# Performance work log

Measured on AMD Instinct MI355X. Metric: run time of the kernel, lower is better.

Reference implementation:

```python
import jax, jax.numpy as jnp
import numpy as np

N = 1147      # 240 lncRNA + 412 disease + 495 miRNA nodes (hard-coded in source)
HID = 512
NH = 8        # heads
P = 73408     # edges (avg degree ~64)
IN_CH = 512


def _ln(x, eps=1e-5):
    m = x.mean(-1, keepdims=True)
    v = ((x - m) ** 2).mean(-1, keepdims=True)
    return (x - m) * jax.lax.rsqrt(v + eps)


def _seg_softmax_agg(logits, v_src, dst, n):
    # logits: [P, NH], v_src: [P, NH, d]; softmax over incoming edges per dst node
    m = jax.ops.segment_max(logits, dst, num_segments=n)
    m = jnp.where(jnp.isfinite(m), m, 0.0)
    a = jnp.exp(logits - m[dst])
    den = jax.ops.segment_sum(a, dst, num_segments=n)
    w = a / (den[dst] + 1e-9)
    return jax.ops.segment_sum(w[..., None] * v_src, dst, num_segments=n)


def _lap_pe(src, dst, n, k):
    # symmetric normalized Laplacian eigenvector positional encoding
    A = jnp.zeros((n, n), jnp.float32).at[src, dst].set(1.0)
    A = jnp.maximum(A, A.T)
    dinv = jax.lax.rsqrt(jnp.maximum(A.sum(1), 1.0))
    L = jnp.eye(n, dtype=jnp.float32) - dinv[:, None] * A * dinv[None, :]
    _, vecs = jnp.linalg.eigh(L)
    return vecs[:, 1:k + 1]  # drop trivial eigenvector


def _edge_layer(h, e, src, dst, Wq, Wk, Wv, We, Wo, Woe, Wfa, Wfb, Wea, Web):
    n, D = h.shape
    d = D // NH
    scale = 1.0 / np.sqrt(d)
    q = (h @ Wq).reshape(n, NH, d)
    k = (h @ Wk).reshape(n, NH, d)
    v = (h @ Wv).reshape(n, NH, d)
    ep = (e @ We).reshape(-1, NH, d)
    score = k[src] * q[dst] * scale * ep           # [P, NH, d]
    e1 = _ln(e + score.reshape(-1, D) @ Woe)       # edge residual path
    e1 = _ln(e1 + jax.nn.relu(e1 @ Wea) @ Web)
    agg = _seg_softmax_agg(score.sum(-1), v[src], dst, n).reshape(n, D)
    h1 = _ln(h + agg @ Wo)
    h1 = _ln(h1 + jax.nn.relu(h1 @ Wfa) @ Wfb)
    return h1, e1


def _gt_layer(h, src, dst, Wq, Wk, Wv, Wo, Wfa, Wfb):
    n, D = h.shape
    d = D // NH
    scale = 1.0 / np.sqrt(d)
    q = (h @ Wq).reshape(n, NH, d)
    k = (h @ Wk).reshape(n, NH, d)
    v = (h @ Wv).reshape(n, NH, d)
    logits = (k[src] * q[dst]).sum(-1) * scale     # [P, NH]
    agg = _seg_softmax_agg(logits, v[src], dst, n).reshape(n, D)
    h1 = _ln(h + agg @ Wo)
    h1 = _ln(h1 + jax.nn.relu(h1 @ Wfa) @ Wfb)
    return h1


def setup_inputs() -> dict:
    key = jax.random.key(0)
    ks = jax.random.split(key, 32)
    s = 0.02
    w = lambda i, shp: jax.random.normal(ks[i], shp, jnp.float32) * s
    return {
        'H': jax.random.normal(ks[0], (N, 1147), jnp.float32),
        'edge_w': jax.random.uniform(ks[1], (P, 1), jnp.float32),
        'edge_src': jax.random.randint(ks[2], (P,), 0, N, jnp.int32),
        'edge_dst': jax.random.randint(ks[3], (P,), 0, N, jnp.int32),
        'W_lin': w(4, (1147, IN_CH)), 'b_lin': jnp.zeros((IN_CH,), jnp.float32),
        'W_e': w(5, (1, HID)), 'b_e': jnp.zeros((HID,), jnp.float32),
        'W_h': w(6, (IN_CH, HID)), 'b_h': jnp.zeros((HID,), jnp.float32),
        'W_lap': w(7, (HID, HID)), 'b_lap': jnp.zeros((HID,), jnp.float32),
        'Wq1': w(8, (HID, HID)), 'Wk1': w(9, (HID, HID)), 'Wv1': w(10, (HID, HID)),
        'We1': w(11, (HID, HID)), 'Wo1': w(12, (HID, HID)), 'Woe1': w(13, (HID, HID)),
        'Wf1a': w(14, (HID, 2 * HID)), 'Wf1b': w(15, (2 * HID, HID)),
        'We1a': w(16, (HID, 2 * HID)), 'We1b': w(17, (2 * HID, HID)),
        'Wq2': w(18, (HID, HID)), 'Wk2': w(19, (HID, HID)), 'Wv2': w(20, (HID, HID)),
        'Wo2': w(21, (HID, HID)),
        'Wf2a': w(22, (HID, 2 * HID)), 'Wf2b': w(23, (2 * HID, HID)),
    }


def reference(H, edge_w, W_lin, b_lin, W_e, b_e, W_h, b_h, W_lap, b_lap,
              Wq1, Wk1, Wv1, We1, Wo1, Woe1, Wf1a, Wf1b, We1a, We1b,
              Wq2, Wk2, Wv2, Wo2, Wf2a, Wf2b, edge_src, edge_dst):
    e = edge_w @ W_e + b_e                       # embedding_e on edge weights
    h = (H @ W_lin + b_lin) @ W_h + b_h          # linear(1147->in_ch) then embedding_h
    pe = _lap_pe(edge_src, edge_dst, N, HID)     # laplacian positional encoding
    h = h + pe @ W_lap + b_lap
    z, _ = _edge_layer(h, e, edge_src, edge_dst, Wq1, Wk1, Wv1, We1,
                       Wo1, Woe1, Wf1a, Wf1b, We1a, We1b)
    z = _gt_layer(z, edge_src, edge_dst, Wq2, Wk2, Wv2, Wo2, Wf2a, Wf2b)
    return z  # [N, HID], already flat per node
```

## Files before the change

### kernel.cpp

```cpp
#include <hip/hip_runtime.h>
#include <hip/hip_cooperative_groups.h>
#include <math.h>

#define NN 1147
#define HID 512
#define LDAe 1152
#define LDQ 1152
#define LDD 1147
#define EPS32 5.9604644775390625e-08f
#define SAFMIN32 1.17549435e-38f
#define I0E 1026
#define TGRID 64
#define TBLK 1024
#define GENSTRIDE 16

struct EDMeta { int K; int nrot; int early; float rho; };
struct ETree { int st[64]; int sz[64]; int cnt; };
struct MergeLvl { int cnt; int st[32]; int n1[32]; int n2[32]; };

__device__ __forceinline__ float lapy2f(float x, float y){
  float xa=fabsf(x), ya=fabsf(y), w=fmaxf(xa,ya), z2=fminf(xa,ya);
  if (z2==0.f) return w;
  float q=z2/w; return w*sqrtf(1.f+q*q);
}
// ... 88 lines not shown
  size_t idx=(size_t)row*LDAe+col;
  float v=A[idx];
  float v1=(dinv[row]*v)*dinv[col];
  float v2=(dinv[col]*v)*dinv[row];
  A[idx] = ((row==col)?1.f:0.f) - 0.5f*(v1+v2);
}

__device__ __forceinline__ float dload(const float* p){
  return __hip_atomic_load(p, __ATOMIC_RELAXED, __HIP_MEMORY_SCOPE_AGENT);
}
__device__ __forceinline__ void dstore(float* p, float v){
  __hip_atomic_store(p, v, __ATOMIC_RELAXED, __HIP_MEMORY_SCOPE_AGENT);
}

__device__ __forceinline__ void gbar(unsigned* flags, unsigned* genrep, unsigned tgt){
  __syncthreads();
  if (threadIdx.x==0)
    __hip_atomic_store(&flags[blockIdx.x], tgt, __ATOMIC_RELAXED, __HIP_MEMORY_SCOPE_AGENT);
  if (blockIdx.x==0){
    if (threadIdx.x<TGRID){
      while (__hip_atomic_load(&flags[threadIdx.x], __ATOMIC_RELAXED, __HIP_MEMORY_SCOPE_AGENT) < tgt)
        __builtin_amdgcn_s_sleep(1);
    }
    __syncthreads();
    if (threadIdx.x<TGRID)
      __hip_atomic_store(&genrep[threadIdx.x*GENSTRIDE], tgt, __ATOMIC_RELAXED, __HIP_MEMORY_SCOPE_AGENT);
  } else {
    if (threadIdx.x==0){
      while (__hip_atomic_load(&genrep[blockIdx.x*GENSTRIDE], __ATOMIC_RELAXED, __HIP_MEMORY_SCOPE_AGENT) < tgt)
        __builtin_amdgcn_s_sleep(1);
    }
    __syncthreads();
  }
}

__global__ __launch_bounds__(1024) void k_trid(float* __restrict__ A, float* __restrict__ evec,
    float* __restrict__ tauv, float* __restrict__ scalv, float* __restrict__ pv2,
    float* __restrict__ pub4, unsigned* __restrict__ flags, unsigned* __restrict__ genrep){
  __shared__ float vbuf[2][1152];
  __shared__ float pcur[1152];
  __shared__ float pubc[1152];
  __shared__ float red[256];
  __shared__ float bcv;
  int tid=threadIdx.x, bid=blockIdx.x;
  int wv=tid>>6, lane=tid&63;
  unsigned tgt=0;
  float tau, scal;
  {
    const float* row0=A;
    int m0=NN-1;
    if (tid<256){
      float s=0.f;
      for(int t=tid;t<m0-1;t+=256){ float x=row0[2+t]; s+=x*x; }
      red[tid]=s;
    }
    float xn2=tree256(red,&bcv,tid);
    float alpha=row0[1];
    float beta;
    if(xn2==0.f){ tau=0.f; beta=alpha; scal=0.f; }
    else { beta=-copysignf(sqrtf(alpha*alpha+xn2),alpha); tau=(beta-alpha)/beta; scal=1.f/(alpha-beta); }
    if(bid==0&&tid==0){ evec[0]=beta; tauv[0]=tau; scalv[0]=scal; }
    for(int t=tid;t<m0;t+=TBLK) vbuf[0][t]=row0[1+t];
    __syncthreads();
    for(int rr=0;rr<2;rr++){
      int r=16*bid+wv+rr*1024;
      if(r<1||r>=NN) continue;
      const float* arow=A+(size_t)r*LDAe+1;
      float acc=0.f;
      for(int c=lane;c<m0;c+=64){
        float v=(c==0)?1.f:vbuf[0][c]*scal;
        acc+=arow[c]*v;
      }
      for(int o=32;o;o>>=1) acc+=__shfl_down(acc,o,64);
      if(lane==0) dstore(&pv2[r],acc);
    }
    if(bid==0&&wv==1){
      const float* r1=A+(size_t)LDAe;
      for(int c=2+lane;c<NN;c+=64) dstore(&pub4[1280+c],r1[c]);
    }
  }
  gbar(flags,genrep,++tgt);
  int cur=0;
  for(int i=0;i<I0E;i++){
    int m=NN-1-i, mp=m-1;
    float* vcur=vbuf[cur]; float* nxt=vbuf[cur^1];
    const float* pvs=pv2+(size_t)(i&1)*1280;
    const float* pbs=pub4+(size_t)((i+1)&3)*1280;
    if (tid<256){
      float s=0.f;
      for(int t=tid;t<m;t+=256){
        float pv=dload(&pvs[(i+1)+t]);
        pcur[t]=pv;
        float v=(t==0)?1.f:vcur[t]*scal;
        s+=pv*v;
      }
      red[tid]=s;
    } else {
      for(int t=tid-256;t<mp;t+=768) pubc[t]=dload(&pbs[(i+2)+t]);
    }
    float sv=tree256(red,&bcv,tid);
    float c2=tau*tau*sv*0.5f;
    const float vz=1.f;
    float wR0=tau*pcur[0]-c2*vz;
    if (tid<256){
      float s2=0.f;
      if (tid==0){
        float vC=vcur[1]*scal;
        float wC=tau*pcur[1]-c2*vC;
        nxt[0]=pubc[0]-(vz*wC+wR0*vC);
      }
      for(int u=tid+1;u<mp;u+=256){
        float vC=vcur[1+u]*scal;
        float wC=tau*pcur[1+u]-c2*vC;
        float x=pubc[u]-(vz*wC+wR0*vC);
        nxt[u]=x;
        s2+=x*x;
      }
      red[tid]=s2;
    }
    float xn2=tree256(red,&bcv,tid);
    float alpha1=nxt[0];
    float beta1,tau1,scal1;
    if(xn2==0.f){ tau1=0.f; beta1=alpha1; scal1=0.f; }
    else { beta1=-copysignf(sqrtf(alpha1*alpha1+xn2),alpha1); tau1=(beta1-alpha1)/beta1; scal1=1.f/(alpha1-beta1); }
    if(bid==0&&tid==0){ evec[i+1]=beta1; tauv[i+1]=tau1; scalv[i+1]=scal1; }
    float* pvd=pv2+(size_t)((i+1)&1)*1280;
    float* pbd=pub4+(size_t)((i+2)&3)*1280;
    for(int rr=0;rr<2;rr++){
      int r=16*bid+wv+rr*1024;
      if(r<i+1||r>=NN) continue;
      int tr=r-(i+1);
      float vR=(tr==0)?1.f:vcur[tr]*scal;
      float wR=tau*pcur[tr]-c2*vR;
      float* arow=A+(size_t)r*LDAe;
      if(lane==0) arow[i+1]=arow[i+1]-(vR*wR0+wR*vz);
      if(tr==0){
        for(int c=lane;c<mp;c+=64) arow[i+2+c]=nxt[c];
      } else {
        float acc=0.f;
        int ispub=(tr==1);
        for(int c=lane;c<mp;c+=64){
          float vC=vcur[1+c]*scal;
          float wC=tau*pcur[1+c]-c2*vC;
          float val=arow[i+2+c]-(vR*wC+wR*vC);
          arow[i+2+c]=val;
          float v1=(c==0)?1.f:nxt[c]*scal1;
          acc+=val*v1;
          if(ispub) dstore(&pbd[(i+2)+c],val);
        }
        for(int o=32;o;o>>=1) acc+=__shfl_down(acc,o,64);
        if(lane==0) dstore(&pvd[r],acc);
      }
    }
    gbar(flags,genrep,++tgt);
    cur^=1; tau=tau1; scal=scal1;
  }
}
__global__ __launch_bounds__(256) void k_tend(float* __restrict__ A, float* __restrict__ evec,
    float* __restrict__ tauv, float* __restrict__ scalv){
  __shared__ float T[121][122];
  __shared__ float red[256];
  __shared__ float bct;
  __shared__ float pl[121];
  __shared__ float el[121], tl[121], sl[121];
  __shared__ float sh3[2];
  int tid=threadIdx.x;
// ... 136 lines not shown
        for(int j2=mm-1;j2>=l;j2--){
          float cc=workc[j2-l], ss2=works[j2-l];
          if (cc!=1.f||ss2!=0.f)
            for(int row=lane;row<n;row+=64){
              float t1=z[(size_t)(j2+1)*ldz+row];
              z[(size_t)(j2+1)*ldz+row]=cc*t1 - ss2*z[(size_t)j2*ldz+row];
              z[(size_t)j2*ldz+row]=ss2*t1 + cc*z[(size_t)j2*ldz+row];
            }
        }
        d[l]=d[l]-p;
        e[l]=g;
      }
    } else {
      for(;;){
        int mm;
        for(mm=l;mm>lend;mm--){
          float tst=e[mm-1]*e[mm-1];
          if (tst<=(eps2*fabsf(d[mm]))*fabsf(d[mm-1])+safmin) break;
        }
        if (mm>lend) e[mm-1]=0.f;
        p=d[l];
        if (mm==l){ d[l]=p; l--; if (l>=lend) continue; else break; }
        if (mm==l-1){
          slaev2(d[l-1],e[l-1],d[l],&rt1,&rt2,&c,&s);
          for(int row=lane;row<n;row+=64){
            float t1=z[(size_t)l*ldz+row];
            z[(size_t)l*ldz+row]=c*t1 - s*z[(size_t)(l-1)*ldz+row];
            z[(size_t)(l-1)*ldz+row]=s*t1 + c*z[(size_t)(l-1)*ldz+row];
          }
          d[l-1]=rt1; d[l]=rt2; e[l-1]=0.f;
          l-=2;
          if (l>=lend) continue; else break;
        }
        if (jtot==nmaxit) break;
        jtot++;
        g=(d[l-1]-p)/(2.f*e[l-1]);
        r=lapy2f(g,1.f);
        g=d[mm]-p+(e[l-1]/(g+copysignf(r,g)));
        s=1.f; c=1.f; p=0.f;
        for(int i=mm;i<=l-1;i++){
          f=s*e[i]; b=c*e[i];
          slartg(g,f,&c,&s,&r);
          if (i!=mm) e[i-1]=r;
          g=d[i]-p;
          r=(d[i+1]-g)*s+2.f*c*b;
          p=s*r;
          d[i]=g+p;
          g=c*r-b;
          workc[i-mm]=c; works[i-mm]=s;
        }
        for(int j2=mm;j2<=l-1;j2++){
          float cc=workc[j2-mm], ss2=works[j2-mm];
          if (cc!=1.f||ss2!=0.f)
            for(int row=lane;row<n;row+=64){
              float t1=z[(size_t)(j2+1)*ldz+row];
              z[(size_t)(j2+1)*ldz+row]=cc*t1 - ss2*z[(size_t)j2*ldz+row];
              z[(size_t)j2*ldz+row]=ss2*t1 + cc*z[(size_t)j2*ldz+row];
            }
        }
        d[l]=d[l]-p;
        e[l-1]=g;
      }
    }
  }
  for(int ii=1;ii<n;ii++){
    int i=ii-1,k=i; float pp=d[i];
    for(int j2=ii;j2<n;j2++) if (d[j2]<pp){k=j2;pp=d[j2];}
    if (k!=i){
      d[k]=d[i]; d[i]=pp;
      for(int row=lane;row<n;row+=64){
        float t1=z[(size_t)i*ldz+row];
        z[(size_t)i*ldz+row]=z[(size_t)k*ldz+row];
        z[(size_t)k*ldz+row]=t1;
      }
    }
  }
}
__global__ __launch_bounds__(64) void k_ed_leaves(float* D, float* E, float* QM, int* indxq, ETree t){
  int lf=blockIdx.x;
  if (lf>=t.cnt) return;
  int lane=threadIdx.x;
  int st=t.st[lf], n=t.sz[lf];
  __shared__ float dl[32], el[32];
  for(int i=lane;i<n;i+=64) dl[i]=D[st+i];
  for(int i=lane;i<n-1;i+=64) el[i]=E[st+i];
  __syncthreads();
  float* z=QM+(size_t)st*LDQ+st;
  for(int c=lane;c<n;c+=64) z[(size_t)c*LDQ+c]=1.f;
  steqr1w(n, dl, el, z, LDQ, lane);
  __syncthreads();
  for(int i=lane;i<n;i+=64){ D[st+i]=dl[i]; indxq[st+i]=i; }
  for(int i=lane;i<n-1;i+=64) E[st+i]=el[i];
}

__global__ __launch_bounds__(256) void k_ed_deflate2(float* __restrict__ D, int* __restrict__ indxq,
    float* __restrict__ dlamda, float* __restrict__ w, float* __restrict__ dstage,
    int* __restrict__ colmap, int* __restrict__ cmtype, int* __restrict__ indxcg,
    int* __restrict__ rotp, int* __restrict__ rotn, float* __restrict__ rotc, float* __restrict__ rots,
    EDMeta* __restrict__ meta, const float* __restrict__ QM, const float* __restrict__ E, MergeLvl lv){
  int mid=blockIdx.x; if(mid>=lv.cnt) return;
  int st=lv.st[mid], n1=lv.n1[mid], n2=lv.n2[mid], n=n1+n2;
  int tid=threadIdx.x;
  __shared__ float zl[1152], dl_[1152], dlam[1152], wl[1152], ds2[1152];
  __shared__ int iq[1152], im[1152], ix[1152], ixp[1152], ict[1152], is2[1152];
  __shared__ float rv[256]; __shared__ int ri[256];
  __shared__ float srho; __shared__ int sK, snrot, searly, simax, sjmax;
  float rr=E[st+n1-1];
  if(tid==0) srho=fabsf(2.f*rr);
  for(int i=tid;i<n;i+=256){
    float v = (i<n1)? QM[(size_t)(st+i)*LDQ + st+n1-1] : QM[(size_t)(st+i)*LDQ + st+n1];
    if(rr<0.f && i>=n1) v=-v;
    zl[i]=v*0.70710678118654752440f;
    dl_[i]=D[st+i];
    int q=indxq[st+i]; if(i>=n1) q+=n1;
    iq[i]=q;
    ict[i]=(i<n1)?1:3;
  }
  __syncthreads();
  {
    float bv=-1.f; int bi=0;
    for(int i2=tid;i2<n;i2+=256){ float a=fabsf(zl[i2]); if(a>bv){bv=a;bi=i2;} }
    rv[tid]=bv; ri[tid]=bi; __syncthreads();
    for(int stp=128;stp;stp>>=1){
      if(tid<stp){ if(rv[tid+stp]>rv[tid]||(rv[tid+stp]==rv[tid]&&ri[tid+stp]<ri[tid])){rv[tid]=rv[tid+stp];ri[tid]=ri[tid+stp];} }
      __syncthreads();
    }
    if(tid==0) simax=ri[0];
    __syncthreads();
  }
  {
    float bv=-1.f; int bi=0;
    for(int i2=tid;i2<n;i2+=256){ float a=fabsf(dl_[i2]); if(a>bv){bv=a;bi=i2;} }
    rv[tid]=bv; ri[tid]=bi; __syncthreads();
    for(int stp=128;stp;stp>>=1){
      if(tid<stp){ if(rv[tid+stp]>rv[tid]||(rv[tid+stp]==rv[tid]&&ri[tid+stp]<ri[tid])){rv[tid]=rv[tid+stp];ri[tid]=ri[tid+stp];} }
      __syncthreads();
    }
    if(tid==0) sjmax=ri[0];
    __syncthreads();
  }
  if(tid==0){
    for(int i=0;i<n;i++) dlam[i]=dl_[iq[i]];
    lamrg0(n1,n2,dlam,1,1,im);
    for(int i=0;i<n;i++) ix[i]=iq[im[i]];
    float tol=8.f*EPS32*fmaxf(fabsf(dl_[sjmax]),fabsf(zl[simax]));
    float rho=srho;
    int K=0,nrot=0,early=0;
    if(rho*fabsf(zl[simax])<=tol){
      early=1;
      for(int i=0;i<n;i++){ int s2=ix[i]; im[i]=s2; iq[i]=2; ds2[i]=dl_[s2]; is2[i]=i; }
    } else {
      int K2=n; int pj=0; int j=0;
      for(;j<n;j++){ int nj=ix[j]; if(rho*fabsf(zl[nj])<=tol){K2--;ict[nj]=4;ixp[K2]=nj;} else {pj=nj;break;} }
      for(j=j+1;;j++){
        if(j>=n) break;
        int nj=ix[j];
        if(rho*fabsf(zl[nj])<=tol){K2--;ict[nj]=4;ixp[K2]=nj;}
        else {
          float s=zl[pj], c=zl[nj];
          float tau2=lapy2f(c,s);
          float t=dl_[nj]-dl_[pj];
          c=c/tau2; s=-s/tau2;
          if(fabsf(t*c*s)<=tol){
            zl[nj]=tau2; zl[pj]=0.f;
            if(ict[nj]!=ict[pj]) ict[nj]=2;
            ict[pj]=4;
            rotp[st+nrot]=pj; rotn[st+nrot]=nj; rotc[st+nrot]=c; rots[st+nrot]=s; nrot++;
            float t2=dl_[pj]*c*c + dl_[nj]*s*s;
            dl_[nj]=dl_[pj]*s*s + dl_[nj]*c*c;
            dl_[pj]=t2;
            K2--;
            int i2=1;
            for(;;){
              if(K2+i2<=n-1 && dl_[pj]<dl_[ixp[K2+i2]]){ ixp[K2+i2-1]=ixp[K2+i2]; ixp[K2+i2]=pj; i2++; }
              else { ixp[K2+i2-1]=pj; break; }
// ... 228 lines not shown
    float* __restrict__ QM, const EDMeta* __restrict__ meta, MergeLvl lv){
  int mid=blockIdx.z; if(mid>=lv.cnt) return;
  int st=lv.st[mid], n=lv.n1[mid]+lv.n2[mid];
  int K=meta[mid].K;
  int br=blockIdx.x*64, bj=blockIdx.y*64;
  if (br>=n||bj>=n) return;
  int tid=threadIdx.x, tr=tid/16, tc=tid%16;
  if (bj>=K){
    for(int i=0;i<4;i++){ int r=br+tr*4+i; if(r>=n)continue;
      for(int j2=0;j2<4;j2++){ int cc=bj+tc*4+j2; if(cc>=n)continue;
        QM[(size_t)(st+cc)*LDQ+st+r]=Q2[(size_t)(st+cc)*LDQ+st+r]; } }
    return;
  }
  __shared__ float As[16][65], Bs[16][65];
  float acc[4][4]={};
  for(int k0=0;k0<K;k0+=16){
    for(int l=0;l<4;l++){
      int e2=tid+l*256;
      int rr=e2&63, ii=e2>>6;
      float av=0.f;
      if (br+rr<n && k0+ii<K) av=Q2[(size_t)(st+k0+ii)*LDQ + st+br+rr];
      As[ii][rr]=av;
      int bi=e2&15, bj2=e2>>4;
      float bv=0.f;
      if (k0+bi<K && bj+bj2<n) bv=DC[(size_t)(st+bj+bj2)*LDD + k0+bi];
      Bs[bi][bj2]=bv;
    }
    __syncthreads();
    #pragma unroll
    for(int kk=0;kk<16;kk++){
      float ar[4],br2[4];
      #pragma unroll
      for(int i=0;i<4;i++) ar[i]=As[kk][tr*4+i];
      #pragma unroll
      for(int j2=0;j2<4;j2++) br2[j2]=Bs[kk][tc*4+j2];
      #pragma unroll
      for(int i=0;i<4;i++)
        #pragma unroll
        for(int j2=0;j2<4;j2++) acc[i][j2]+=ar[i]*br2[j2];
    }
    __syncthreads();
  }
  for(int i=0;i<4;i++){
    int r=br+tr*4+i; if (r>=n) continue;
    for(int j2=0;j2<4;j2++){
      int cc=bj+tc*4+j2; if (cc>=n) continue;
      if (cc<K) QM[(size_t)(st+cc)*LDQ + st+r]=acc[i][j2];
      else      QM[(size_t)(st+cc)*LDQ + st+r]=Q2[(size_t)(st+cc)*LDQ + st+r];
    }
  }
}
__global__ __launch_bounds__(256) void k_ed_post(float* __restrict__ D, const float* __restrict__ dstage,
    int* __restrict__ indxq, const EDMeta* __restrict__ meta, MergeLvl lv){
  int mid=blockIdx.x; if(mid>=lv.cnt) return;
  int st=lv.st[mid], n=lv.n1[mid]+lv.n2[mid];
  int K=meta[mid].K;
  int tid=threadIdx.x;
  __shared__ float dl[1152];
  __shared__ int iq[1152];
  float* Ds=D+st;
  for(int i=tid;i<n;i+=256){
    float v = (i<K)? Ds[i] : dstage[st+i];
    dl[i]=v;
    if (i>=K) Ds[i]=v;
  }
  __syncthreads();
  if (meta[mid].early){
    for(int i=tid;i<n;i+=256) indxq[st+i]=i;
    return;
  }
  if (tid==0) lamrg0(K, n-K, dl, 1, -1, iq);
  __syncthreads();
  for(int i=tid;i<n;i+=256) indxq[st+i]=iq[i];
}
__global__ __launch_bounds__(256) void k_ed_gather(const float* __restrict__ QM, const int* __restrict__ indxq,
    float* __restrict__ Vt){
  int row=blockIdx.x*256+threadIdx.x;
  int vec=blockIdx.y;
  if (row>=NN) return;
  int src=indxq[vec+1];
  Vt[(size_t)vec*NN+row]=QM[(size_t)src*LDQ+row];
}

__global__ __launch_bounds__(256) void k_backt(const float* __restrict__ A, const float* __restrict__ tauv,
                                               const float* __restrict__ scalv, float* __restrict__ Vt){
  __shared__ float cols[4][1168];
  __shared__ float tl[1152], sl[1152];
  int wv=threadIdx.x>>6, lane=threadIdx.x&63;
  int vec=blockIdx.x*4+wv;
  float* col=Vt+(size_t)vec*NN;
  float* cl=cols[wv];
  for(int t=threadIdx.x;t<NN;t+=256){ tl[t]=tauv[t]; sl[t]=scalv[t]; }
  for(int t=lane;t<NN;t+=64) cl[t]=col[t];
  __syncthreads();
  for(int i=NN-2;i>=0;i--){
    float tau=tl[i];
    if (tau==0.f) continue;
    int m=NN-1-i;
    float scal=sl[i];
    const float* rowi=A+(size_t)i*LDAe;
    float s=0.f;
    for(int t=lane;t<m;t+=64){
      float v=(t==0)?1.f:rowi[i+1+t]*scal;
      s+=v*cl[i+1+t];
    }
    for(int o=32;o;o>>=1) s+=__shfl_down(s,o,64);
    s=__shfl(s,0,64);
    s*=tau;
    for(int t=lane;t<m;t+=64){
      float v=(t==0)?1.f:rowi[i+1+t]*scal;
      cl[i+1+t]-=s*v;
    }
  }
  for(int t=lane;t<NN;t+=64) col[t]=cl[t];
}

__global__ __launch_bounds__(256) void k_transpose(const float* __restrict__ in, float* __restrict__ outp){
  __shared__ float tile[32][33];
  int c0=blockIdx.x*32, r0=blockIdx.y*32;
  int tx=threadIdx.x%32, ty=threadIdx.x/32;
  for(int s=0;s<32;s+=8){
    int r=r0+ty+s, c=c0+tx;
    tile[ty+s][tx]=(r<512 && c<NN)? in[(size_t)r*NN+c] : 0.f;
  }
  __syncthreads();
  for(int s=0;s<32;s+=8){
    int r=c0+ty+s, c=r0+tx;
    if (r<NN && c<512) outp[(size_t)r*512+c]=tile[tx][ty+s];
  }
}

__global__ __launch_bounds__(256) void k_gemm(const float* __restrict__ A, const float* __restrict__ B,
    const float* __restrict__ bias, const float* __restrict__ add, float* __restrict__ C,
    int M, int Nc, int K, int relu){
  __shared__ float As[16][65];
  __shared__ float Bs[16][65];
  int bm=blockIdx.y*64, bn=blockIdx.x*64;
  int tid=threadIdx.x;
  int tr=tid/16, tc=tid%16;
  float acc[4][4]={};
  for(int k0=0;k0<K;k0+=16){
    for(int l=0;l<4;l++){
      int e2=tid+l*256;
      int m_=e2/16, kk=e2%16;
      float av=0.f;
      if (bm+m_<M && k0+kk<K) av=A[(size_t)(bm+m_)*K + k0+kk];
      As[kk][m_]=av;
      int k2=e2/64, n2=e2%64;
      float bv=0.f;
      if (k0+k2<K && bn+n2<Nc) bv=B[(size_t)(k0+k2)*Nc + bn+n2];
      Bs[k2][n2]=bv;
    }
    __syncthreads();
    for(int kk=0;kk<16;kk++){
      float ar[4], br[4];
      #pragma unroll
      for(int i=0;i<4;i++) ar[i]=As[kk][tr*4+i];
      #pragma unroll
      for(int j=0;j<4;j++) br[j]=Bs[kk][tc*4+j];
      #pragma unroll
      for(int i=0;i<4;i++)
        #pragma unroll
        for(int j=0;j<4;j++) acc[i][j]+=ar[i]*br[j];
    }
    __syncthreads();
  }
  for(int i=0;i<4;i++){
    int r=bm+tr*4+i;
    if (r>=M) continue;
    for(int j=0;j<4;j++){
      int c=bn+tc*4+j;
      if (c>=Nc) continue;
      float x=acc[i][j];
      if (bias) x+=bias[c];
      if (add)  x+=add[(size_t)r*Nc+c];
      if (relu) x=fmaxf(x,0.f);
      C[(size_t)r*Nc+c]=x;
    }
  }
}

__global__ __launch_bounds__(256) void k_lnadd(const float* __restrict__ x, const float* __restrict__ y,
                                               float* __restrict__ out){
  int row=blockIdx.x; int tid=threadIdx.x;
  __shared__ float red[256];
  size_t base=(size_t)row*HID;
  float v0=x[base+tid]+y[base+tid];
  float v1=x[base+256+tid]+y[base+256+tid];
  red[tid]=v0+v1; __syncthreads();
  for(int st=128;st;st>>=1){ if(tid<st) red[tid]+=red[tid+st]; __syncthreads(); }
  float mean=red[0]*(1.f/512.f);
  __syncthreads();
  float d0=v0-mean, d1=v1-mean;
  red[tid]=d0*d0+d1*d1; __syncthreads();
  for(int st=128;st;st>>=1){ if(tid<st) red[tid]+=red[tid+st]; __syncthreads(); }
  float r=rsqrtf(red[0]*(1.f/512.f)+1e-5f);
  out[base+tid]=d0*r;
  out[base+256+tid]=d1*r;
}

__global__ __launch_bounds__(256) void k_prep_uw(const float* __restrict__ We, const float* __restrict__ be,
    const float* __restrict__ We1, float* __restrict__ u, float* __restrict__ w1){
  int c=blockIdx.x*256+threadIdx.x;
  if (c>=HID) return;
  float a=0.f,b=0.f;
  for(int f=0;f<HID;f++){ float m=We1[(size_t)f*HID+c]; a+=We[f]*m; b+=be[f]*m; }
  u[c]=a; w1[c]=b;
}

__global__ __launch_bounds__(256) void k_elogits(const float* __restrict__ q, const float* __restrict__ kk,
    const int* __restrict__ src, const int* __restrict__ dst, const float* __restrict__ ew,
    const float* __restrict__ uu, const float* __restrict__ ww, float* __restrict__ logit, int P, int useep){
  int gw=(blockIdx.x*256+threadIdx.x)>>6;
  int lane=threadIdx.x&63;
  if (gw>=P) return;
  int s=src[gw], d=dst[gw];
  const float* kr=kk+(size_t)s*HID;
  const float* qr=q+(size_t)d*HID;
  float a1[8], a2[8];
  #pragma unroll
  for(int j=0;j<8;j++){
    int c=j*64+lane;
    float prod=kr[c]*qr[c];
    if (useep){ a1[j]=prod*uu[c]; a2[j]=prod*ww[c]; }
    else { a1[j]=prod; a2[j]=0.f; }
  }
  #pragma unroll
  for(int o=32;o;o>>=1){
    #pragma unroll
    for(int j=0;j<8;j++){ a1[j]+=__shfl_down(a1[j],o,64); a2[j]+=__shfl_down(a2[j],o,64); }
  }
  if (lane==0){
    float w0 = useep? ew[gw] : 0.f;
    #pragma unroll
    for(int j=0;j<8;j++){
      float lg = useep ? 0.125f*(w0*a1[j]+a2[j]) : 0.125f*a1[j];
      logit[(size_t)gw*8+j]=lg;
    }
  }
}

__global__ __launch_bounds__(256) void k_count(const int* __restrict__ dst, int* __restrict__ cnt, int P){
  int p=blockIdx.x*256+threadIdx.x;
  if (p<P) atomicAdd(&cnt[dst[p]],1);
}
__global__ __launch_bounds__(256) void k_scan(const int* __restrict__ cnt, int* __restrict__ iptr){
  __shared__ int c[NN+1];
  int tid=threadIdx.x;
  for(int i=tid;i<NN;i+=256) c[i]=cnt[i];
  __syncthreads();
  if (tid==0){
    int s=0;
    for(int n=0;n<NN;n++){ int t=c[n]; c[n]=s; s+=t; }
    c[NN]=s;
  }
  __syncthreads();
  for(int i=tid;i<=NN;i+=256) iptr[i]=c[i];
}
__global__ __launch_bounds__(256) void k_fill(const int* __restrict__ dst, const int* __restrict__ iptr,
                                              int* __restrict__ iidx, int P){
// ... 135 lines not shown
  int* rotp=AI(1280); int* rotn=AI(1280);
  EDMeta* meta=(EDMeta*)AI(192);
  int* icnt=AI(NN); int* iptr=AI(NN+1); int* iidx=AI(P);
  int* barws=AI(2048);
  unsigned* flags=(unsigned*)barws;
  unsigned* genrep=(unsigned*)(barws+64);
  (void)ws_size; (void)n_in; (void)out_size;

  float* W0=A;        float* W1=A+SLOT;
  float* W2=QM;       float* W3=QM+SLOT;
  float* W4=Q2;       float* W5=Q2+SLOT;
  float* W6=DC;       float* W7=DC+SLOT;
  (void)W7;
  float* Vt=W6;
  float* pe=W2;

  auto GEMM=[&](const float*Am,const float*Bm,const float*bias,const float*add,float*C,int M,int Nc,int K,int relu){
    dim3 g((Nc+63)/64,(M+63)/64);
    k_gemm<<<g,256,0,stream>>>(Am,Bm,bias,add,C,M,Nc,K,relu);
  };

  {
    int ntot=NN*LDAe;
    k_zero_f<<<(ntot+255)/256,256,0,stream>>>(A,ntot);
    k_adj<<<(P+255)/256,256,0,stream>>>(esrc,edst,A,P);
    k_deg<<<NN,256,0,stream>>>(A,pvec);
    dim3 g((NN+255)/256,NN);
    k_lap<<<g,256,0,stream>>>(A,pvec);
  }
  k_zero_i<<<8,256,0,stream>>>(barws,2048);
  {
    void* kargs[] = { (void*)&A, (void*)&evec, (void*)&tauv, (void*)&scalv,
                      (void*)&pv2, (void*)&pub4, (void*)&flags, (void*)&genrep };
    hipLaunchCooperativeKernel((const void*)k_trid, dim3(TGRID), dim3(TBLK), kargs, 0, stream);
  }
  k_tend<<<1,256,0,stream>>>(A,evec,tauv,scalv);
  k_harvest<<<(NN+255)/256,256,0,stream>>>(A,dvec);

  ETree tr;
  {
    int tmp[64]; tmp[0]=NN; int cnt=1;
    while (tmp[cnt-1]>25){
      for(int j2=cnt-1;j2>=0;j2--){ int p=tmp[j2]; tmp[2*j2]=p/2; tmp[2*j2+1]=p-p/2; }
      cnt*=2;
    }
    tr.cnt=cnt;
    int acc=0;
    for(int j2=0;j2<cnt;j2++){ tr.st[j2]=acc; tr.sz[j2]=tmp[j2]; acc+=tmp[j2]; }
  }
  k_ed_scale<<<1,256,0,stream>>>(dvec,evec);
  k_zero_f<<<(LDQ*NN+255)/256,256,0,stream>>>(QM,LDQ*NN);
  k_ed_cuts<<<1,64,0,stream>>>(dvec,evec,tr);
  k_ed_leaves<<<tr.cnt,64,0,stream>>>(dvec,evec,QM,indxq,tr);

  {
    int csz[64], cst[64], cn=tr.cnt;
    for(int i=0;i<cn;i++){ csz[i]=tr.sz[i]; cst[i]=tr.st[i]; }
    while (cn>1){
      MergeLvl lv; lv.cnt=cn/2;
      int maxn=0;
      for(int i=0;i<cn/2;i++){
        lv.st[i]=cst[2*i]; lv.n1[i]=csz[2*i]; lv.n2[i]=csz[2*i+1];
        int n=lv.n1[i]+lv.n2[i]; if(n>maxn) maxn=n;
      }
      k_ed_deflate2<<<lv.cnt,256,0,stream>>>(dvec,indxq,eddl,edw,edds,edcm,edcmt,edic,
                                             rotp,rotn,rotc,rots,meta,QM,evec,lv);
      { dim3 gr((maxn+255)/256,lv.cnt);
        k_ed_rot2<<<gr,256,0,stream>>>(QM,rotp,rotn,rotc,rots,meta,lv); }
      { dim3 gp((maxn+255)/256,maxn,lv.cnt);
        k_ed_permute<<<gp,256,0,stream>>>(QM,Q2,edcm,edcmt,lv); }
      { dim3 gs((maxn+63)/64,lv.cnt);
        k_ed_secular<<<gs,64,0,stream>>>(eddl,edw,meta,dvec,DC,lv);
        k_ed_lowner<<<gs,64,0,stream>>>(eddl,edw,DC,meta,lv); }
      { dim3 gv(maxn,lv.cnt);
        k_ed_vecs<<<gv,256,0,stream>>>(edw,DC,edic,meta,lv); }
      { dim3 gg((maxn+63)/64,(maxn+63)/64,lv.cnt);
        k_gemm_cm2<<<gg,256,0,stream>>>(Q2,DC,QM,meta,lv); }
      k_ed_post<<<lv.cnt,256,0,stream>>>(dvec,edds,indxq,meta,lv);
      for(int i=0;i<cn/2;i++){ cst[i]=cst[2*i]; csz[i]=csz[2*i]+csz[2*i+1]; }
      cn>>=1;
    }
  }
  { dim3 gg((NN+255)/256,512); k_ed_gather<<<gg,256,0,stream>>>(QM,indxq,Vt); }
  k_backt<<<128,256,0,stream>>>(A,tauv,scalv,Vt);
  { dim3 g((NN+31)/32,(512+31)/32); k_transpose<<<g,256,0,stream>>>(Vt,pe); }

  float* hx=W0; float* h0=W1; float* hb=W4;
  GEMM(H,W_lin,b_lin,nullptr,hx,NN,HID,NN,0);
  GEMM(hx,W_h,b_h,nullptr,h0,NN,HID,HID,0);
  GEMM(pe,W_lap,b_lap,h0,hb,NN,HID,HID,0);
  k_prep_uw<<<2,256,0,stream>>>(W_e,b_e,We1,ub,w1b);
  k_zero_i<<<(NN+255)/256,256,0,stream>>>(icnt,NN);
  k_count<<<(P+255)/256,256,0,stream>>>(edst,icnt,P);
  k_scan<<<1,256,0,stream>>>(icnt,iptr);
  k_fill<<<NN,256,0,stream>>>(edst,iptr,iidx,P);
  float* qb=W0; float* kb=W1; float* vb=W3;
  GEMM(hb,Wq1,nullptr,nullptr,qb,NN,HID,HID,0);
  GEMM(hb,Wk1,nullptr,nullptr,kb,NN,HID,HID,0);
  GEMM(hb,Wv1,nullptr,nullptr,vb,NN,HID,HID,0);
  float* logit=W2;
  k_elogits<<<(P+3)/4,256,0,stream>>>(qb,kb,esrc,edst,edge_w,ub,w1b,logit,P,1);
  float* wght=W5;
  k_softmax<<<NN,256,0,stream>>>(logit,iptr,iidx,wght);
  float* aggb=W6;
  k_agg<<<NN,512,0,stream>>>(wght,vb,esrc,iptr,iidx,aggb);
  float* ob=W0;
  GEMM(aggb,Wo1,nullptr,nullptr,ob,NN,HID,HID,0);
  float* h1a=W3;
  k_lnadd<<<NN,256,0,stream>>>(hb,ob,h1a);
  float* tb1=W0;
  GEMM(h1a,Wf1a,nullptr,nullptr,tb1,NN,1024,HID,1);
  float* fb=W2;
  GEMM(tb1,Wf1b,nullptr,nullptr,fb,NN,HID,1024,0);
  float* h1=W5;
  k_lnadd<<<NN,256,0,stream>>>(h1a,fb,h1);
  float* q2=W0; float* k2=W1; float* v2=W2;
  GEMM(h1,Wq2,nullptr,nullptr,q2,NN,HID,HID,0);
  GEMM(h1,Wk2,nullptr,nullptr,k2,NN,HID,HID,0);
  GEMM(h1,Wv2,nullptr,nullptr,v2,NN,HID,HID,0);
  float* logit2=W3;
  k_elogits<<<(P+3)/4,256,0,stream>>>(q2,k2,esrc,edst,nullptr,nullptr,nullptr,logit2,P,0);
  float* wght2=W4;
  k_softmax<<<NN,256,0,stream>>>(logit2,iptr,iidx,wght2);
  float* agg2=W6;
  k_agg<<<NN,512,0,stream>>>(wght2,v2,esrc,iptr,iidx,agg2);
  float* o2=W0;
  GEMM(agg2,Wo2,nullptr,nullptr,o2,NN,HID,HID,0);
  float* h2a=W1;
  k_lnadd<<<NN,256,0,stream>>>(h1,o2,h2a);
  float* tb2=W2;
  GEMM(h2a,Wf2a,nullptr,nullptr,tb2,NN,1024,HID,1);
  float* f2=W0;
  GEMM(tb2,Wf2b,nullptr,nullptr,f2,NN,HID,1024,0);
  k_lnadd<<<NN,256,0,stream>>>(h2a,f2,out);
}
```

Baseline: 28.42 ms.

## Retire idle tridiagonalization blocks early, localize leaf eigensolve, fuse QKV GEMMs

Measured after the change: 28.30 ms. Within noise of the previous version (-0.4%).

```diff
diff --git a/kernel.cpp b/kernel.cpp
--- a/kernel.cpp
+++ b/kernel.cpp
@@ -194,6 +194,11 @@
   gbar(flags,genrep,++tgt);
   int cur=0;
   for(int i=0;i<I0E;i++){
+    if (bid>=8 && i>=16*bid+15){
+      if (tid==0)
+        __hip_atomic_store(&flags[bid], 0x7FFFFFFFu, __ATOMIC_RELAXED, __HIP_MEMORY_SCOPE_AGENT);
+      return;
+    }
     int m=NN-1-i, mp=m-1;
     float* vcur=vbuf[cur]; float* nxt=vbuf[cur^1];
     const float* pvs=pv2+(size_t)(i&1)*1280;
@@ -496,15 +501,16 @@
   int lane=threadIdx.x;
   int st=t.st[lf], n=t.sz[lf];
   __shared__ float dl[32], el[32];
+  __shared__ float zloc[32][33];
   for(int i=lane;i<n;i+=64) dl[i]=D[st+i];
   for(int i=lane;i<n-1;i+=64) el[i]=E[st+i];
-  __syncthreads();
-  float* z=QM+(size_t)st*LDQ+st;
-  for(int c=lane;c<n;c+=64) z[(size_t)c*LDQ+c]=1.f;
-  steqr1w(n, dl, el, z, LDQ, lane);
+  for(int e=lane;e<n*n;e+=64){ int c=e/n, r=e%n; zloc[c][r]=(c==r)?1.f:0.f; }
+  __syncthreads();
+  steqr1w(n, dl, el, &zloc[0][0], 33, lane);
   __syncthreads();
   for(int i=lane;i<n;i+=64){ D[st+i]=dl[i]; indxq[st+i]=i; }
   for(int i=lane;i<n-1;i+=64) E[st+i]=el[i];
+  for(int e=lane;e<n*n;e+=64){ int c=e/n, r=e%n; QM[(size_t)(st+c)*LDQ + st+r]=zloc[c][r]; }
 }
 
 __global__ __launch_bounds__(256) void k_ed_deflate2(float* __restrict__ D, int* __restrict__ indxq,
@@ -899,15 +905,15 @@
   Vt[(size_t)vec*NN+row]=QM[(size_t)src*LDQ+row];
 }
 
-__global__ __launch_bounds__(256) void k_backt(const float* __restrict__ A, const float* __restrict__ tauv,
+__global__ __launch_bounds__(128) void k_backt(const float* __restrict__ A, const float* __restrict__ tauv,
                                                const float* __restrict__ scalv, float* __restrict__ Vt){
-  __shared__ float cols[4][1168];
+  __shared__ float cols[2][1168];
   __shared__ float tl[1152], sl[1152];
   int wv=threadIdx.x>>6, lane=threadIdx.x&63;
-  int vec=blockIdx.x*4+wv;
+  int vec=blockIdx.x*2+wv;
   float* col=Vt+(size_t)vec*NN;
   float* cl=cols[wv];
-  for(int t=threadIdx.x;t<NN;t+=256){ tl[t]=tauv[t]; sl[t]=scalv[t]; }
+  for(int t=threadIdx.x;t<NN;t+=128){ tl[t]=tauv[t]; sl[t]=scalv[t]; }
   for(int t=lane;t<NN;t+=64) cl[t]=col[t];
   __syncthreads();
   for(int i=NN-2;i>=0;i--){
@@ -993,6 +999,62 @@
       if (add)  x+=add[(size_t)r*Nc+c];
       if (relu) x=fmaxf(x,0.f);
       C[(size_t)r*Nc+c]=x;
+    }
+  }
+}
+
+__global__ __launch_bounds__(256) void k_gemm3(const float* __restrict__ A,
+    const float* __restrict__ B0, const float* __restrict__ B1, const float* __restrict__ B2,
+    float* __restrict__ C0, float* __restrict__ C1, float* __restrict__ C2,
+    int M, int Nc, int K){
+  __shared__ float As[16][65];
+  __shared__ float Bs[3][16][65];
+  int bm=blockIdx.y*64, bn=blockIdx.x*64;
+  int tid=threadIdx.x;
+  int tr=tid/16, tc=tid%16;
+  float acc[3][4][4]={};
+  const float* Bp0=B0; const float* Bp1=B1; const float* Bp2=B2;
+  for(int k0=0;k0<K;k0+=16){
+    for(int l=0;l<4;l++){
+      int e2=tid+l*256;
+      int m_=e2/16, kk=e2%16;
+      float av=0.f;
+      if (bm+m_<M && k0+kk<K) av=A[(size_t)(bm+m_)*K + k0+kk];
+      As[kk][m_]=av;
+      int k2=e2/64, n2=e2%64;
+      bool ok=(k0+k2<K && bn+n2<Nc);
+      size_t bidx=(size_t)(k0+k2)*Nc + bn+n2;
+      Bs[0][k2][n2]= ok? Bp0[bidx]:0.f;
+      Bs[1][k2][n2]= ok? Bp1[bidx]:0.f;
+      Bs[2][k2][n2]= ok? Bp2[bidx]:0.f;
+    }
+    __syncthreads();
+    for(int kk=0;kk<16;kk++){
+      float ar[4];
+      #pragma unroll
+      for(int i=0;i<4;i++) ar[i]=As[kk][tr*4+i];
+      #pragma unroll
+      for(int q=0;q<3;q++){
+        float br[4];
+        #pragma unroll
+        for(int j=0;j<4;j++) br[j]=Bs[q][kk][tc*4+j];
+        #pragma unroll
+        for(int i=0;i<4;i++)
+          #pragma unroll
+          for(int j=0;j<4;j++) acc[q][i][j]+=ar[i]*br[j];
+      }
+    }
+    __syncthreads();
+  }
+  for(int i=0;i<4;i++){
+    int r=bm+tr*4+i;
+    if (r>=M) continue;
+    for(int j=0;j<4;j++){
+      int c=bn+tc*4+j;
+      if (c>=Nc) continue;
+      C0[(size_t)r*Nc+c]=acc[0][i][j];
+      C1[(size_t)r*Nc+c]=acc[1][i][j];
+      C2[(size_t)r*Nc+c]=acc[2][i][j];
     }
   }
 }
@@ -1294,7 +1356,7 @@
     }
   }
   { dim3 gg((NN+255)/256,512); k_ed_gather<<<gg,256,0,stream>>>(QM,indxq,Vt); }
-  k_backt<<<128,256,0,stream>>>(A,tauv,scalv,Vt);
+  k_backt<<<256,128,0,stream>>>(A,tauv,scalv,Vt);
   { dim3 g((NN+31)/32,(512+31)/32); k_transpose<<<g,256,0,stream>>>(Vt,pe); }
 
   float* hx=W0; float* h0=W1; float* hb=W4;
@@ -1307,9 +1369,8 @@
   k_scan<<<1,256,0,stream>>>(icnt,iptr);
   k_fill<<<NN,256,0,stream>>>(edst,iptr,iidx,P);
   float* qb=W0; float* kb=W1; float* vb=W3;
-  GEMM(hb,Wq1,nullptr,nullptr,qb,NN,HID,HID,0);
-  GEMM(hb,Wk1,nullptr,nullptr,kb,NN,HID,HID,0);
-  GEMM(hb,Wv1,nullptr,nullptr,vb,NN,HID,HID,0);
+  { dim3 g((HID+63)/64,(NN+63)/64);
+    k_gemm3<<<g,256,0,stream>>>(hb,Wq1,Wk1,Wv1,qb,kb,vb,NN,HID,HID); }
   float* logit=W2;
   k_elogits<<<(P+3)/4,256,0,stream>>>(qb,kb,esrc,edst,edge_w,ub,w1b,logit,P,1);
   float* wght=W5;
@@ -1327,9 +1388,8 @@
   float* h1=W5;
   k_lnadd<<<NN,256,0,stream>>>(h1a,fb,h1);
   float* q2=W0; float* k2=W1; float* v2=W2;
-  GEMM(h1,Wq2,nullptr,nullptr,q2,NN,HID,HID,0);
-  GEMM(h1,Wk2,nullptr,nullptr,k2,NN,HID,HID,0);
-  GEMM(h1,Wv2,nullptr,nullptr,v2,NN,HID,HID,0);
+  { dim3 g((HID+63)/64,(NN+63)/64);
+    k_gemm3<<<g,256,0,stream>>>(h1,Wq2,Wk2,Wv2,q2,k2,v2,NN,HID,HID); }
   float* logit2=W3;
   k_elogits<<<(P+3)/4,256,0,stream>>>(q2,k2,esrc,edst,nullptr,nullptr,nullptr,logit2,P,0);
   float* wght2=W4;
```
